# Optimization experiments

Measured on AMD Instinct MI355X. Metric: run time of the kernel, lower is better.

## Reference

```python
import jax, jax.numpy as jnp
import numpy as np

B, L1, L2, D1, D2 = 32, 2048, 2048, 1024, 1024


def setup_inputs() -> dict:
    key = jax.random.key(0)
    k1, k2, k3 = jax.random.split(key, 3)
    x1 = jax.random.normal(k1, (B, L1, D1), dtype=jnp.float32)
    x2 = jax.random.normal(k2, (B, L2, D2), dtype=jnp.float32)
    # xavier_normal_ init for U [dim1, dim2]
    std = float(np.sqrt(2.0 / (D1 + D2)))
    U = jax.random.normal(k3, (D1, D2), dtype=jnp.float32) * std
    return {"x1": x1, "x2": x2, "U": U}


def reference(x1, x2, U):
    # M[b,i,j] = x1[b,i,:] @ U @ x2[b,j,:]  -> [B, L1, L2]
    M = jnp.einsum('bid,de,bje->bij', x1, U, x2)
    # row attention: max over L2 then softmax over L1 -> [B, L1]
    rows = jax.nn.softmax(M.max(axis=2), axis=1)
    # col attention: max over L1 then softmax over L2 -> [B, L2]
    cols = jax.nn.softmax(M.max(axis=1), axis=1)
    _x1 = jnp.einsum('bi,bid->bd', rows, x1)  # [B, D1]
    _x2 = jnp.einsum('bj,bjd->bd', cols, x2)  # [B, D2]
    return (_x1, _x2)
```

## Files before the change

### kernel.cpp

```cpp
#include <hip/hip_runtime.h>
#include <hip/hip_bf16.h>
#include <stdint.h>

#define B_  32
#define L_  2048
#define D_  1024

typedef __attribute__((ext_vector_type(8))) _Float16 f16x8;
typedef __attribute__((ext_vector_type(4))) float f32x4;

__device__ __forceinline__ unsigned enc_f(float x) {
  unsigned u = __float_as_uint(x);
  return (u & 0x80000000u) ? ~u : (u | 0x80000000u);
}
__device__ __forceinline__ float dec_f(unsigned e) {
  unsigned u = (e & 0x80000000u) ? (e ^ 0x80000000u) : ~e;
  return __uint_as_float(u);
}
__device__ __forceinline__ ushort f16_bits(float x) {
  _Float16 h = (_Float16)x;
  return __builtin_bit_cast(ushort, h);
}
__device__ __forceinline__ void split_f16(float x, ushort& h, ushort& l) {
  _Float16 hf = (_Float16)x;
  float r = x - (float)hf;
  h = __builtin_bit_cast(ushort, hf);
  l = __builtin_bit_cast(ushort, (_Float16)r);
}

__device__ __forceinline__ void gl_lds16(const ushort* g, ushort* l) {
  using gas_t = const __attribute__((address_space(1))) uint32_t*;
  using las_t = __attribute__((address_space(3))) uint32_t*;
  __builtin_amdgcn_global_load_lds((gas_t)(uintptr_t)g,
                                   (las_t)(unsigned)(uintptr_t)l, 16, 0, 0);
}

__global__ void dec1_k(const float4* __restrict__ x, uint2* __restrict__ h, int n4) {
  int i = blockIdx.x * blockDim.x + threadIdx.x;
  const int stride = gridDim.x * blockDim.x;
  for (; i < n4; i += stride) {
    float4 v = x[i];
    uint2 hw;
    hw.x = (unsigned)f16_bits(v.x) | ((unsigned)f16_bits(v.y) << 16);
    hw.y = (unsigned)f16_bits(v.z) | ((unsigned)f16_bits(v.w) << 16);
    h[i] = hw;
  }
}

__global__ void transdec_k(const float* __restrict__ U,
                           ushort* __restrict__ UTh, ushort* __restrict__ UTl) {
  __shared__ float t[32][33];
  const int tx = threadIdx.x, ty = threadIdx.y;
  const int e0 = blockIdx.x * 32, d0 = blockIdx.y * 32;
#pragma unroll
  for (int r = 0; r < 4; ++r)
    t[ty + r * 8][tx] = U[(size_t)(d0 + ty + r * 8) * D_ + e0 + tx];
  __syncthreads();
#pragma unroll
  for (int r = 0; r < 4; ++r) {
    int e = ty + r * 8;
    ushort h, l;
    split_f16(t[tx][e] * 2048.0f, h, l);
    UTh[(size_t)(e0 + e) * D_ + d0 + tx] = h;
    UTl[(size_t)(e0 + e) * D_ + d0 + tx] = l;
  }
}

struct CoreCtx {
  int w, lane, ln, kq, wm, wn, ko;
  size_t soA;
};

__device__ __forceinline__ CoreCtx make_ctx() {
  CoreCtx c;
  const int tid = threadIdx.x;
  c.w = tid >> 6; c.lane = tid & 63;
  c.ln = c.lane & 15; c.kq = c.lane >> 4;
  c.wm = c.w >> 2; c.wn = c.w & 3;
  c.ko = (c.kq ^ ((c.ln >> 1) & 3)) * 8;
  const int srow = c.lane >> 2;
  const int sslot = (c.lane & 3) ^ ((c.lane >> 3) & 3);
  c.soA = (size_t)(c.w * 32 + srow) * D_ + sslot * 8;
  return c;
}

__device__ __forceinline__ void stage_plane(const ushort* src, ushort* dstbase,
                                            const CoreCtx& c, int k0) {
  const size_t a0 = c.soA + k0, a1 = a0 + (size_t)16 * D_;
  ushort* d0 = dstbase + c.w * 1024;
  gl_lds16(src + a0, d0);
  gl_lds16(src + a1, d0 + 512);
}

#define VMCNT(n) asm volatile("s_waitcnt vmcnt(" #n ")" ::: "memory")
#define BARRIER() do { asm volatile("" ::: "memory"); \
                       __builtin_amdgcn_s_barrier();  \
                       asm volatile("" ::: "memory"); } while (0)

__device__ __forceinline__ void core_loop3(const CoreCtx& c,
    const ushort* Ah, const ushort* Bh, const ushort* Bl,
    ushort* lbuf, f32x4 acc[8][4])
{
  stage_plane(Ah, lbuf,         c, 0);
  stage_plane(Bh, lbuf + 8192,  c, 0);
  stage_plane(Bl, lbuf + 16384, c, 0);

  for (int t = 0; t < 32; ++t) {
    const ushort* cb = lbuf + (t & 1) * 24576;
    ushort* nb = lbuf + ((t + 1) & 1) * 24576;
    const int kn = (t + 1) * 32;
    const bool pf = (t < 31);
    f16x8 a[8], bh4[4], bl4[4];

    VMCNT(2);
    BARRIER();
#pragma unroll
    for (int n = 0; n < 4; ++n) {
      const int r = c.wn * 64 + n * 16 + c.ln;
      bh4[n] = *(const f16x8*)&cb[8192 + r * 32 + c.ko];
    }
#pragma unroll
    for (int m = 0; m < 8; ++m) {
      const int r = c.wm * 128 + m * 16 + c.ln;
      a[m] = *(const f16x8*)&cb[r * 32 + c.ko];
    }
    if (pf) { stage_plane(Ah, nb, c, kn); stage_plane(Bh, nb + 8192, c, kn); }
    __builtin_amdgcn_s_setprio(1);
#pragma unroll
    for (int m = 0; m < 8; ++m)
#pragma unroll
      for (int n = 0; n < 4; ++n)
        acc[m][n] = __builtin_amdgcn_mfma_f32_16x16x32_f16(a[m], bh4[n], acc[m][n], 0, 0, 0);
    __builtin_amdgcn_s_setprio(0);

    if (pf) { VMCNT(4); } else { VMCNT(0); }
    BARRIER();
#pragma unroll
    for (int n = 0; n < 4; ++n) {
      const int r = c.wn * 64 + n * 16 + c.ln;
      bl4[n] = *(const f16x8*)&cb[16384 + r * 32 + c.ko];
    }
    if (pf) stage_plane(Bl, nb + 16384, c, kn);
    __builtin_amdgcn_s_setprio(1);
#pragma unroll
    for (int m = 0; m < 8; ++m)
#pragma unroll
      for (int n = 0; n < 4; ++n)
        acc[m][n] = __builtin_amdgcn_mfma_f32_16x16x32_f16(a[m], bl4[n], acc[m][n], 0, 0, 0);
    __builtin_amdgcn_s_setprio(0);
  }
}

__global__ __launch_bounds__(512, 2) void gemm1_k(
    const ushort* __restrict__ x1h,
    const ushort* __restrict__ UTh, const ushort* __restrict__ UTl,
    ushort* __restrict__ Yh)
{
  __shared__ __attribute__((aligned(16))) ushort lbuf[65536];
  const int z = blockIdx.z;
  const int orig = blockIdx.x;
  const int xc = orig & 7, j = orig >> 3;
  const int bx = (xc & 3) * 2 + (j & 1);
  const int by = (xc >> 2) * 2 + (j >> 1);

  const size_t zb = (size_t)z * (L_ * D_);
  const ushort* Ah = x1h + zb + (size_t)bx * 256 * D_;
  const ushort* Bh = UTh + (size_t)by * 256 * D_;
  const ushort* Bl = UTl + (size_t)by * 256 * D_;

  CoreCtx c = make_ctx();
  f32x4 acc[8][4];
#pragma unroll
  for (int m = 0; m < 8; ++m)
#pragma unroll
    for (int n = 0; n < 4; ++n) acc[m][n] = (f32x4){0.f, 0.f, 0.f, 0.f};

  core_loop3(c, Ah, Bh, Bl, lbuf, acc);

  __syncthreads();

  ushort* ep = lbuf + c.w * 8192;
  const int grow = bx * 256 + c.wm * 128;
  const int gcol = by * 256 + c.wn * 64;
#pragma unroll
  for (int m = 0; m < 8; ++m)
#pragma unroll
    for (int n = 0; n < 4; ++n)
#pragma unroll
      for (int r2 = 0; r2 < 4; ++r2) {
        float v = acc[m][n][r2] * 4.8828125e-4f;
        ep[(m * 16 + c.kq * 4 + r2) * 64 + n * 16 + c.ln] = f16_bits(v);
      }
#pragma unroll
  for (int q = 0; q < 16; ++q) {
    const int chunk = q * 64 + c.lane;
    const int row = chunk >> 3, c8 = (chunk & 7) * 8;
    f16x8 v = *(const f16x8*)&ep[row * 64 + c8];
    *(f16x8*)&Yh[zb + (size_t)(grow + row) * D_ + gcol + c8] = v;
  }
}

__global__ __launch_bounds__(512, 2) void gemm2_k(
    const ushort* __restrict__ Yh,
    const ushort* __restrict__ x2h,
    unsigned* __restrict__ rmxg, unsigned* __restrict__ cmxg)
{
  __shared__ __attribute__((aligned(16))) ushort lbuf[32768];
  const int z = blockIdx.z;
  const int orig = blockIdx.x;
  const int xc = orig & 7, j = orig >> 3;
  const int bx = (xc & 3) * 2 + (j & 1);
  const int by = (xc >> 2) * 4 + (j >> 1);

  const size_t zb = (size_t)z * (L_ * D_);
  const ushort* Ah = Yh + zb + (size_t)bx * 256 * D_;
  const ushort* Bh = x2h + zb + (size_t)by * 256 * D_;

  CoreCtx c = make_ctx();
  f32x4 acc[8][4];
#pragma unroll
  for (int m = 0; m < 8; ++m)
#pragma unroll
    for (int n = 0; n < 4; ++n) acc[m][n] = (f32x4){0.f, 0.f, 0.f, 0.f};

  stage_plane(Ah, lbuf,        c, 0);
  stage_plane(Bh, lbuf + 8192, c, 0);

  for (int t = 0; t < 32; ++t) {
    const ushort* cb = lbuf + (t & 1) * 16384;
    ushort* nb = lbuf + ((t + 1) & 1) * 16384;
    if (t < 31) {
      const int kn = (t + 1) * 32;
      stage_plane(Ah, nb, c, kn);
      stage_plane(Bh, nb + 8192, c, kn);
      VMCNT(4);
    } else {
      VMCNT(0);
    }
    BARRIER();
    f16x8 a[8], bh4[4];
#pragma unroll
    for (int n = 0; n < 4; ++n) {
      const int r = c.wn * 64 + n * 16 + c.ln;
      bh4[n] = *(const f16x8*)&cb[8192 + r * 32 + c.ko];
    }
#pragma unroll
    for (int m = 0; m < 8; ++m) {
      const int r = c.wm * 128 + m * 16 + c.ln;
      a[m] = *(const f16x8*)&cb[r * 32 + c.ko];
    }
    __builtin_amdgcn_s_setprio(1);
#pragma unroll
    for (int m = 0; m < 8; ++m)
#pragma unroll
      for (int n = 0; n < 4; ++n)
        acc[m][n] = __builtin_amdgcn_mfma_f32_16x16x32_f16(a[m], bh4[n], acc[m][n], 0, 0, 0);
    __builtin_amdgcn_s_setprio(0);
    BARRIER();
  }

  __syncthreads();
  unsigned* red = (unsigned*)lbuf;
  const int tid = threadIdx.x;
  red[tid] = 0u;
  __syncthreads();

#pragma unroll
  for (int m = 0; m < 8; ++m) {
#pragma unroll
    for (int r2 = 0; r2 < 4; ++r2) {
      float v = fmaxf(fmaxf(acc[m][0][r2], acc[m][1][r2]),
                      fmaxf(acc[m][2][r2], acc[m][3][r2]));
#pragma unroll
      for (int s = 1; s < 16; s <<= 1) v = fmaxf(v, __shfl_xor(v, s));
      if (c.ln == 0) atomicMax(&red[c.wm * 128 + m * 16 + c.kq * 4 + r2], enc_f(v));
    }
  }
#pragma unroll
  for (int n = 0; n < 4; ++n) {
    float v = -3.4e38f;
#pragma unroll
    for (int m = 0; m < 8; ++m)
#pragma unroll
      for (int r2 = 0; r2 < 4; ++r2) v = fmaxf(v, acc[m][n][r2]);
    v = fmaxf(v, __shfl_xor(v, 16));
    v = fmaxf(v, __shfl_xor(v, 32));
    if (c.kq == 0) atomicMax(&red[256 + c.wn * 64 + n * 16 + c.ln], enc_f(v));
  }
  __syncthreads();
  if (tid < 256) atomicMax(&rmxg[(size_t)z * L_ + bx * 256 + tid], red[tid]);
  else           atomicMax(&cmxg[(size_t)z * L_ + by * 256 + (tid - 256)], red[tid]);
}

__global__ void softmax_k(const unsigned* __restrict__ enc, float* __restrict__ w) {
  __shared__ float red[256];
  const int b = blockIdx.x, tid = threadIdx.x;
  const unsigned* e = enc + (size_t)b * L_;
  float* wb = w + (size_t)b * L_;
  float vals[8];
  float lmax = -3.4e38f;
#pragma unroll
  for (int q = 0; q < 8; ++q) {
    float f = dec_f(e[q * 256 + tid]);
    vals[q] = f;
    lmax = fmaxf(lmax, f);
  }
  red[tid] = lmax; __syncthreads();
  for (int s = 128; s > 0; s >>= 1) {
    if (tid < s) red[tid] = fmaxf(red[tid], red[tid + s]);
    __syncthreads();
  }
  const float mx = red[0];
  __syncthreads();
  float lsum = 0.f;
#pragma unroll
  for (int q = 0; q < 8; ++q) { vals[q] = expf(vals[q] - mx); lsum += vals[q]; }
  red[tid] = lsum; __syncthreads();
  for (int s = 128; s > 0; s >>= 1) {
    if (tid < s) red[tid] += red[tid + s];
    __syncthreads();
  }
  const float inv = 1.f / red[0];
#pragma unroll
  for (int q = 0; q < 8; ++q) wb[q * 256 + tid] = vals[q] * inv;
}

__global__ void wsum_k(const float* __restrict__ w, const ushort* __restrict__ xh,
                       float* __restrict__ out) {
  __shared__ float ws[256];
  const int tid = threadIdx.x;
  const int b = blockIdx.y;
  const int i0 = blockIdx.x * 256;
  ws[tid] = w[(size_t)b * L_ + i0 + tid];
  __syncthreads();
  const int d0 = tid * 4;
  const ushort* xb = xh + ((size_t)b * L_ + i0) * D_ + d0;
  float4 acc = {0.f, 0.f, 0.f, 0.f};
  for (int i = 0; i < 256; ++i) {
    ushort4 v = *(const ushort4*)(xb + (size_t)i * D_);
    float wi = ws[i];
    acc.x = fmaf(wi, (float)__builtin_bit_cast(_Float16, v.x), acc.x);
    acc.y = fmaf(wi, (float)__builtin_bit_cast(_Float16, v.y), acc.y);
    acc.z = fmaf(wi, (float)__builtin_bit_cast(_Float16, v.z), acc.z);
    acc.w = fmaf(wi, (float)__builtin_bit_cast(_Float16, v.w), acc.w);
  }
  float* o = out + (size_t)b * D_ + d0;
  atomicAdd(o + 0, acc.x);
  atomicAdd(o + 1, acc.y);
  atomicAdd(o + 2, acc.z);
  atomicAdd(o + 3, acc.w);
}

extern "C" void kernel_launch(void* const* d_in, const int* in_sizes, int n_in,
                              void* d_out, int out_size, void* d_ws, size_t ws_size,
                              hipStream_t stream) {
  (void)in_sizes; (void)n_in; (void)out_size;
  const float* x1 = (const float*)d_in[0];
  const float* x2 = (const float*)d_in[1];
  const float* U  = (const float*)d_in[2];
  float* out = (float*)d_out;

  char* p = (char*)d_ws;
  ushort* UTh = (ushort*)p; p += (size_t)D_ * D_ * 2;
  ushort* UTl = (ushort*)p; p += (size_t)D_ * D_ * 2;
  unsigned* rowmax = (unsigned*)p; p += (size_t)B_ * L_ * 4;
  unsigned* colmax = (unsigned*)p; p += (size_t)B_ * L_ * 4;
  float* w1 = (float*)p; p += (size_t)B_ * L_ * 4;
  float* w2 = (float*)p; p += (size_t)B_ * L_ * 4;
  const size_t fixed = (size_t)(p - (char*)d_ws);
  const size_t perB = (size_t)3 * L_ * D_ * 2;
  int G = 1;
  if (ws_size > fixed) {
    size_t g = (ws_size - fixed) / perB;
    G = g < 1 ? 1 : (g > (size_t)B_ ? B_ : (int)g);
  }
  ushort* x1h = (ushort*)p;
  ushort* x2h = x1h + (size_t)G * L_ * D_;
  ushort* Yh  = x2h + (size_t)G * L_ * D_;

  hipMemsetAsync(d_out, 0, (size_t)2 * B_ * D_ * 4, stream);
  hipMemsetAsync(rowmax, 0, (size_t)2 * B_ * L_ * 4, stream);

  transdec_k<<<dim3(32, 32), dim3(32, 8), 0, stream>>>(U, UTh, UTl);

  for (int g0 = 0; g0 < B_; g0 += G) {
    const int Gc = (B_ - g0) < G ? (B_ - g0) : G;
    const int n4 = Gc * (L_ * D_ / 4);
    dec1_k<<<dim3(1024), 256, 0, stream>>>(
        (const float4*)(x1 + (size_t)g0 * L_ * D_), (uint2*)x1h, n4);
    dec1_k<<<dim3(1024), 256, 0, stream>>>(
        (const float4*)(x2 + (size_t)g0 * L_ * D_), (uint2*)x2h, n4);
    gemm1_k<<<dim3(32, 1, Gc), 512, 0, stream>>>(x1h, UTh, UTl, Yh);
    gemm2_k<<<dim3(64, 1, Gc), 512, 0, stream>>>(Yh, x2h,
        rowmax + (size_t)g0 * L_, colmax + (size_t)g0 * L_);
    softmax_k<<<dim3(Gc), 256, 0, stream>>>(rowmax + (size_t)g0 * L_,
                                            w1 + (size_t)g0 * L_);
    softmax_k<<<dim3(Gc), 256, 0, stream>>>(colmax + (size_t)g0 * L_,
                                            w2 + (size_t)g0 * L_);
    wsum_k<<<dim3(8, Gc), 256, 0, stream>>>(w1 + (size_t)g0 * L_, x1h,
                                            out + (size_t)g0 * D_);
    wsum_k<<<dim3(8, Gc), 256, 0, stream>>>(w2 + (size_t)g0 * L_, x2h,
                                            out + (size_t)(B_ + g0) * D_);
  }
}
```

Measured before the change: 745.5 us.

## Quad-buffer gemm2 K-loop and prefetch LDS fragments ahead of MFMA

The gemm2 main loop moves from double-buffered LDS to a four-slot ring. The loop is unrolled by two and register-double-buffers the A/B fragments, so LDS reads for the next K-step are issued before the MFMAs of the current step. sched_barrier markers keep the compiler from reordering these phases. The aim is to hide LDS read latency and global-load latency behind MFMA work. The cost is doubled shared memory (128KB) and more live fragment registers, which may cut occupancy below the two blocks per CU the launch bounds declare.

```diff
diff --git a/kernel.cpp b/kernel.cpp
--- a/kernel.cpp
+++ b/kernel.cpp
@@ -97,6 +97,32 @@
                        __builtin_amdgcn_s_barrier();  \
                        asm volatile("" ::: "memory"); } while (0)
 
+#define READ_FRAGS(cb, Aa, Bb)                                   \
+  do {                                                           \
+    _Pragma("unroll")                                            \
+    for (int n_ = 0; n_ < 4; ++n_) {                             \
+      const int r_ = c.wn * 64 + n_ * 16 + c.ln;                 \
+      Bb[n_] = *(const f16x8*)&(cb)[8192 + r_ * 32 + c.ko];      \
+    }                                                            \
+    _Pragma("unroll")                                            \
+    for (int m_ = 0; m_ < 8; ++m_) {                             \
+      const int r_ = c.wm * 128 + m_ * 16 + c.ln;                \
+      Aa[m_] = *(const f16x8*)&(cb)[r_ * 32 + c.ko];             \
+    }                                                            \
+  } while (0)
+
+#define MFMA32(Aa, Bb)                                                        \
+  do {                                                                       \
+    __builtin_amdgcn_s_setprio(1);                                           \
+    _Pragma("unroll")                                                        \
+    for (int m_ = 0; m_ < 8; ++m_)                                           \
+      _Pragma("unroll")                                                      \
+      for (int n_ = 0; n_ < 4; ++n_)                                         \
+        acc[m_][n_] = __builtin_amdgcn_mfma_f32_16x16x32_f16(Aa[m_], Bb[n_], \
+                                                             acc[m_][n_], 0, 0, 0); \
+    __builtin_amdgcn_s_setprio(0);                                           \
+  } while (0)
+
 __device__ __forceinline__ void core_loop3(const CoreCtx& c,
     const ushort* Ah, const ushort* Bh, const ushort* Bl,
     ushort* lbuf, f32x4 acc[8][4])
@@ -205,7 +231,7 @@
     const ushort* __restrict__ x2h,
     unsigned* __restrict__ rmxg, unsigned* __restrict__ cmxg)
 {
-  __shared__ __attribute__((aligned(16))) ushort lbuf[32768];
+  __shared__ __attribute__((aligned(16))) ushort lbuf[65536];
   const int z = blockIdx.z;
   const int orig = blockIdx.x;
   const int xc = orig & 7, j = orig >> 3;
@@ -223,41 +249,45 @@
 #pragma unroll
     for (int n = 0; n < 4; ++n) acc[m][n] = (f32x4){0.f, 0.f, 0.f, 0.f};
 
-  stage_plane(Ah, lbuf,        c, 0);
-  stage_plane(Bh, lbuf + 8192, c, 0);
-
-  for (int t = 0; t < 32; ++t) {
-    const ushort* cb = lbuf + (t & 1) * 16384;
-    ushort* nb = lbuf + ((t + 1) & 1) * 16384;
-    if (t < 31) {
-      const int kn = (t + 1) * 32;
-      stage_plane(Ah, nb, c, kn);
-      stage_plane(Bh, nb + 8192, c, kn);
-      VMCNT(4);
-    } else {
-      VMCNT(0);
-    }
+  ushort* q0 = lbuf;
+  ushort* q1 = lbuf + 16384;
+  ushort* q2 = lbuf + 32768;
+  ushort* q3 = lbuf + 49152;
+
+  f16x8 aA[8], bA[4], aB[8], bB[4];
+
+  stage_plane(Ah, q0, c, 0);  stage_plane(Bh, q0 + 8192, c, 0);
+  stage_plane(Ah, q1, c, 32); stage_plane(Bh, q1 + 8192, c, 32);
+  VMCNT(4);
+  BARRIER();
+  READ_FRAGS(q0, aA, bA);
+  __builtin_amdgcn_sched_barrier(0);
+
+  for (int tp = 0; tp < 15; ++tp) {
+    const int t0 = 2 * tp;
+    stage_plane(Ah, q2, c, (t0 + 2) * 32);
+    stage_plane(Bh, q2 + 8192, c, (t0 + 2) * 32);
+    VMCNT(4);
     BARRIER();
-    f16x8 a[8], bh4[4];
-#pragma unroll
-    for (int n = 0; n < 4; ++n) {
-      const int r = c.wn * 64 + n * 16 + c.ln;
-      bh4[n] = *(const f16x8*)&cb[8192 + r * 32 + c.ko];
-    }
-#pragma unroll
-    for (int m = 0; m < 8; ++m) {
-      const int r = c.wm * 128 + m * 16 + c.ln;
-      a[m] = *(const f16x8*)&cb[r * 32 + c.ko];
-    }
-    __builtin_amdgcn_s_setprio(1);
-#pragma unroll
-    for (int m = 0; m < 8; ++m)
-#pragma unroll
-      for (int n = 0; n < 4; ++n)
-        acc[m][n] = __builtin_amdgcn_mfma_f32_16x16x32_f16(a[m], bh4[n], acc[m][n], 0, 0, 0);
-    __builtin_amdgcn_s_setprio(0);
+    READ_FRAGS(q1, aB, bB);
+    __builtin_amdgcn_sched_barrier(0);
+    MFMA32(aA, bA);
+    stage_plane(Ah, q3, c, (t0 + 3) * 32);
+    stage_plane(Bh, q3 + 8192, c, (t0 + 3) * 32);
+    VMCNT(4);
     BARRIER();
-  }
+    READ_FRAGS(q2, aA, bA);
+    __builtin_amdgcn_sched_barrier(0);
+    MFMA32(aB, bB);
+    ushort* r0 = q0; ushort* r1 = q1;
+    q0 = q2; q1 = q3; q2 = r0; q3 = r1;
+  }
+  VMCNT(0);
+  BARRIER();
+  READ_FRAGS(q1, aB, bB);
+  __builtin_amdgcn_sched_barrier(0);
+  MFMA32(aA, bA);
+  MFMA32(aB, bB);
 
   __syncthreads();
   unsigned* red = (unsigned*)lbuf;
```

Measured after the change: 724.7 us. 2.8% less time.

## Restructure gemm2 main loop with K=64 tiles and interleaved prefetch/MFMA phases

Applied to the files above, without the earlier changes.

The gemm2 kernel now stages K=64 slices per iteration (16 iterations instead of 32) into a doubled 128KB LDS double buffer, using a new XOR-swizzled layout. Each iteration is split into four MFMA sub-phases, and the global-to-LDS prefetch of each half-tile is issued between them, separated by sched barriers. This halves the barrier count and spreads memory issue across compute to hide latency. The cost is that 128KB of LDS per block probably breaks the 2-blocks-per-CU occupancy target, and VMCNT(0) at the end of each iteration serialises on the prefetch.

```diff
diff --git a/kernel.cpp b/kernel.cpp
--- a/kernel.cpp
+++ b/kernel.cpp
@@ -205,7 +205,7 @@
     const ushort* __restrict__ x2h,
     unsigned* __restrict__ rmxg, unsigned* __restrict__ cmxg)
 {
-  __shared__ __attribute__((aligned(16))) ushort lbuf[32768];
+  __shared__ __attribute__((aligned(16))) ushort lbuf[65536];
   const int z = blockIdx.z;
   const int orig = blockIdx.x;
   const int xc = orig & 7, j = orig >> 3;
@@ -213,55 +213,118 @@
   const int by = (xc >> 2) * 4 + (j >> 1);
 
   const size_t zb = (size_t)z * (L_ * D_);
-  const ushort* Ah = Yh + zb + (size_t)bx * 256 * D_;
-  const ushort* Bh = x2h + zb + (size_t)by * 256 * D_;
-
-  CoreCtx c = make_ctx();
+  const ushort* Ap = Yh + zb + (size_t)bx * 256 * D_;
+  const ushort* Bp = x2h + zb + (size_t)by * 256 * D_;
+
+  const int tid = threadIdx.x;
+  const int w = tid >> 6, lane = tid & 63;
+  const int ln = lane & 15, kq = lane >> 4;
+  const int wm = w >> 2, wn = w & 3;
+  const int ko0 = ((kq)     ^ (ln & 7)) * 8;
+  const int ko1 = ((4 + kq) ^ (ln & 7)) * 8;
+  const int srow8 = lane >> 3;
+  const int sslot8 = (lane & 7) ^ srow8;
+  const size_t sOff = (size_t)(w * 16 + srow8) * D_ + sslot8 * 8;
+
   f32x4 acc[8][4];
 #pragma unroll
   for (int m = 0; m < 8; ++m)
 #pragma unroll
     for (int n = 0; n < 4; ++n) acc[m][n] = (f32x4){0.f, 0.f, 0.f, 0.f};
 
-  stage_plane(Ah, lbuf,        c, 0);
-  stage_plane(Bh, lbuf + 8192, c, 0);
-
-  for (int t = 0; t < 32; ++t) {
-    const ushort* cb = lbuf + (t & 1) * 16384;
-    ushort* nb = lbuf + ((t + 1) & 1) * 16384;
-    if (t < 31) {
-      const int kn = (t + 1) * 32;
-      stage_plane(Ah, nb, c, kn);
-      stage_plane(Bh, nb + 8192, c, kn);
-      VMCNT(4);
-    } else {
-      VMCNT(0);
-    }
+  const ushort* srcH0 = Ap;
+  const ushort* srcH1 = Ap + (size_t)128 * D_;
+  const ushort* srcH2 = Bp;
+  const ushort* srcH3 = Bp + (size_t)128 * D_;
+
+#define STAGE_H(nb, hbase, srcp, kt)                                   \
+  do {                                                                 \
+    const size_t a_ = sOff + (size_t)(kt) * 64;                        \
+    ushort* d_ = (nb) + (hbase) + w * 1024;                            \
+    gl_lds16((srcp) + a_, d_);                                         \
+    gl_lds16((srcp) + a_ + (size_t)8 * D_, d_ + 512);                  \
+  } while (0)
+
+  STAGE_H(lbuf, 0,     srcH0, 0);
+  STAGE_H(lbuf, 8192,  srcH1, 0);
+  STAGE_H(lbuf, 16384, srcH2, 0);
+  STAGE_H(lbuf, 24576, srcH3, 0);
+  VMCNT(0);
+  BARRIER();
+
+  for (int t = 0; t < 16; ++t) {
+    const ushort* cb = lbuf + (t & 1) * 32768;
+    ushort* nb = lbuf + ((t + 1) & 1) * 32768;
+    const bool pf = (t < 15);
+    const int kn = t + 1;
+    const ushort* aB = cb + wm * 8192;
+    const ushort* bB = cb + 16384 + (wn >> 1) * 8192;
+    const int rB = (wn & 1) * 64;
+
+    f16x8 aX[4], aY[4], b0[4], b1[4];
+
+#pragma unroll
+    for (int n = 0; n < 4; ++n)
+      b0[n] = *(const f16x8*)&bB[(rB + n * 16 + ln) * 64 + ko0];
+#pragma unroll
+    for (int m = 0; m < 4; ++m)
+      aX[m] = *(const f16x8*)&aB[(m * 16 + ln) * 64 + ko0];
+    if (pf) STAGE_H(nb, 0, srcH0, kn);
+    __builtin_amdgcn_s_setprio(1);
+#pragma unroll
+    for (int m = 0; m < 4; ++m)
+#pragma unroll
+      for (int n = 0; n < 4; ++n)
+        acc[m][n] = __builtin_amdgcn_mfma_f32_16x16x32_f16(aX[m], b0[n], acc[m][n], 0, 0, 0);
+    __builtin_amdgcn_s_setprio(0);
+    __builtin_amdgcn_sched_barrier(0);
+
+#pragma unroll
+    for (int m = 0; m < 4; ++m)
+      aY[m] = *(const f16x8*)&aB[((64 + m * 16 + ln)) * 64 + ko0];
+    if (pf) STAGE_H(nb, 8192, srcH1, kn);
+    __builtin_amdgcn_s_setprio(1);
+#pragma unroll
+    for (int m = 0; m < 4; ++m)
+#pragma unroll
+      for (int n = 0; n < 4; ++n)
+        acc[4 + m][n] = __builtin_amdgcn_mfma_f32_16x16x32_f16(aY[m], b0[n], acc[4 + m][n], 0, 0, 0);
+    __builtin_amdgcn_s_setprio(0);
+    __builtin_amdgcn_sched_barrier(0);
+
+#pragma unroll
+    for (int n = 0; n < 4; ++n)
+      b1[n] = *(const f16x8*)&bB[(rB + n * 16 + ln) * 64 + ko1];
+#pragma unroll
+    for (int m = 0; m < 4; ++m)
+      aX[m] = *(const f16x8*)&aB[(m * 16 + ln) * 64 + ko1];
+    if (pf) { STAGE_H(nb, 16384, srcH2, kn); STAGE_H(nb, 24576, srcH3, kn); }
+    __builtin_amdgcn_s_setprio(1);
+#pragma unroll
+    for (int m = 0; m < 4; ++m)
+#pragma unroll
+      for (int n = 0; n < 4; ++n)
+        acc[m][n] = __builtin_amdgcn_mfma_f32_16x16x32_f16(aX[m], b1[n], acc[m][n], 0, 0, 0);
+    __builtin_amdgcn_s_setprio(0);
+    __builtin_amdgcn_sched_barrier(0);
+
+#pragma unroll
+    for (int m = 0; m < 4; ++m)
+      aY[m] = *(const f16x8*)&aB[((64 + m * 16 + ln)) * 64 + ko1];
+    __builtin_amdgcn_s_setprio(1);
+#pragma unroll
+    for (int m = 0; m < 4; ++m)
+#pragma unroll
+      for (int n = 0; n < 4; ++n)
+        acc[4 + m][n] = __builtin_amdgcn_mfma_f32_16x16x32_f16(aY[m], b1[n], acc[4 + m][n], 0, 0, 0);
+    __builtin_amdgcn_s_setprio(0);
+
+    if (pf) { VMCNT(0); }
     BARRIER();
-    f16x8 a[8], bh4[4];
-#pragma unroll
-    for (int n = 0; n < 4; ++n) {
-      const int r = c.wn * 64 + n * 16 + c.ln;
-      bh4[n] = *(const f16x8*)&cb[8192 + r * 32 + c.ko];
-    }
-#pragma unroll
-    for (int m = 0; m < 8; ++m) {
-      const int r = c.wm * 128 + m * 16 + c.ln;
-      a[m] = *(const f16x8*)&cb[r * 32 + c.ko];
-    }
-    __builtin_amdgcn_s_setprio(1);
-#pragma unroll
-    for (int m = 0; m < 8; ++m)
-#pragma unroll
-      for (int n = 0; n < 4; ++n)
-        acc[m][n] = __builtin_amdgcn_mfma_f32_16x16x32_f16(a[m], bh4[n], acc[m][n], 0, 0, 0);
-    __builtin_amdgcn_s_setprio(0);
-    BARRIER();
   }
 
   __syncthreads();
   unsigned* red = (unsigned*)lbuf;
-  const int tid = threadIdx.x;
   red[tid] = 0u;
   __syncthreads();
 
@@ -273,7 +336,7 @@
                       fmaxf(acc[m][2][r2], acc[m][3][r2]));
 #pragma unroll
       for (int s = 1; s < 16; s <<= 1) v = fmaxf(v, __shfl_xor(v, s));
-      if (c.ln == 0) atomicMax(&red[c.wm * 128 + m * 16 + c.kq * 4 + r2], enc_f(v));
+      if (ln == 0) atomicMax(&red[wm * 128 + m * 16 + kq * 4 + r2], enc_f(v));
     }
   }
 #pragma unroll
@@ -285,11 +348,12 @@
       for (int r2 = 0; r2 < 4; ++r2) v = fmaxf(v, acc[m][n][r2]);
     v = fmaxf(v, __shfl_xor(v, 16));
     v = fmaxf(v, __shfl_xor(v, 32));
-    if (c.kq == 0) atomicMax(&red[256 + c.wn * 64 + n * 16 + c.ln], enc_f(v));
+    if (kq == 0) atomicMax(&red[256 + wn * 64 + n * 16 + ln], enc_f(v));
   }
   __syncthreads();
   if (tid < 256) atomicMax(&rmxg[(size_t)z * L_ + bx * 256 + tid], red[tid]);
   else           atomicMax(&cmxg[(size_t)z * L_ + by * 256 + (tid - 256)], red[tid]);
+#undef STAGE_H
 }
 
 __global__ void softmax_k(const unsigned* __restrict__ enc, float* __restrict__ w) {
```

Result: faster. 720.5 us (-3.4%).
